# Kernel tuning notes

Hardware: AMD Instinct MI355X
Metric: run time of the kernel (lower is better)

Reference implementation:

```python
import jax, jax.numpy as jnp
import numpy as np

# corner enumeration order matches the original list comprehension:
# (0,0,0),(0,0,d),(0,h,0),(0,h,d),(w,0,0),(w,0,d),(w,h,0),(w,h,d)
CORNER_OFFS = jnp.array([[0,0,0],[0,0,1],[0,1,0],[0,1,1],
                         [1,0,0],[1,0,1],[1,1,0],[1,1,1]], dtype=jnp.float32)
# axis_combinations in original: (i,j) with j>=i over 3 axes -> 6 combos
CROSS_A = jnp.array([0,0,0,1,1,2])
CROSS_B = jnp.array([0,1,2,1,2,2])


def setup_inputs() -> dict:
    key = jax.random.key(0)
    k1, k2, k3 = jax.random.split(key, 3)
    B = 1024
    bb = jax.random.uniform(k1, (B, 6), dtype=jnp.float32)
    rotations = jax.random.normal(k2, (B, 3, 3), dtype=jnp.float32)
    translations = jax.random.normal(k3, (B, 1, 3), dtype=jnp.float32)
    return {"bb": bb, "rotations": rotations, "translations": translations}


def _pv_loss(bb, rotations, translations):
    B = bb.shape[0]
    # [B,8,3] axis-aligned corners, then rotate (corners @ R) and translate
    corners = bb[:, None, :3] + bb[:, None, 3:] * CORNER_OFFS
    corners_t = jnp.einsum('bkd,bde->bke', corners, rotations) + translations
    # unit_vectors is the 3x3 identity, so I @ R == R
    uvt = rotations  # [B,3,3] rows are the transformed unit vectors

    ii, jj = jnp.triu_indices(B, k=1)  # all pairs j > i, P = B(B-1)/2
    c1 = corners_t[ii]  # [P,8,3]
    c2 = corners_t[jj]  # [P,8,3]
    u1 = uvt[ii]        # [P,3,3]
    u2 = uvt[jj]        # [P,3,3]

    # NOTE: the original second axis-loop also uses unit_vector_first[i]
    # (a bug we replicate): the 3 face axes of the FIRST box are tested twice;
    # duplicates do not change min() or the all-intersect decision, so we test
    # them once. Cross axes use the j>=i combinations.
    face_axes = u1                                           # [P,3,3]
    cross_axes = jnp.cross(u1[:, CROSS_A, :], u2[:, CROSS_B, :])  # [P,6,3]
    axes = jnp.concatenate([face_axes, cross_axes], axis=1)  # [P,9,3]
    # original skips exactly-zero cross axes (torch.equal with zeros)
    valid = jnp.concatenate(
        [jnp.ones(face_axes.shape[:2], dtype=bool),
         jnp.any(cross_axes != 0, axis=-1)], axis=1)         # [P,9]

    # SAT projections: dot every corner with every axis
    d1 = jnp.einsum('pkc,pac->pak', c1, axes)  # [P,9,8]
    d2 = jnp.einsum('pkc,pac->pak', c2, axes)  # [P,9,8]
    min1, max1 = d1.min(-1), d1.max(-1)
    min2, max2 = d2.min(-1), d2.max(-1)
    total_len = jnp.maximum(max1, max2) - jnp.minimum(min1, min2)
    sum_len = (max1 - min1) + (max2 - min2)
    overlap = sum_len - total_len                 # [P,9]

    axis_pass = jnp.where(valid, total_len < sum_len, True)
    pair_pass = jnp.all(axis_pass, axis=-1)       # [P]
    overlap_masked = jnp.where(valid, overlap, jnp.inf)
    penalty = jnp.where(pair_pass, overlap_masked.min(-1), 0.0)
    return penalty.sum()


def reference(bb, rotations, translations):
    return _pv_loss(bb, rotations, translations)
```

## Files before the change

### kernel.cpp

```cpp
#include <hip/hip_runtime.h>
#include <hip/hip_bf16.h>

#define NI 8

__device__ __forceinline__ void load_box(const float* __restrict__ bb,
                                         const float* __restrict__ rot,
                                         const float* __restrict__ tr,
                                         int b, float* R, float* p, float* e) {
    const float* s = bb + b * 6;
    const float* r = rot + b * 9;
    const float* t = tr + b * 3;
    float mn0 = s[0], mn1 = s[1], mn2 = s[2];
    float d0 = s[3], d1 = s[4], d2 = s[5];
#pragma unroll
    for (int k = 0; k < 9; k++) R[k] = r[k];
#pragma unroll
    for (int k = 0; k < 3; k++) {
        p[k]     = mn0 * R[k] + mn1 * R[3 + k] + mn2 * R[6 + k] + t[k];
        e[k]     = d0 * R[k];
        e[3 + k] = d1 * R[3 + k];
        e[6 + k] = d2 * R[6 + k];
    }
}

__device__ __forceinline__ float axis_overlap(float ax, float ay, float az,
                                              const float* pi, const float* ei,
                                              const float* pj, const float* ej) {
    float b1 = pi[0] * ax + pi[1] * ay + pi[2] * az;
    float u0 = ei[0] * ax + ei[1] * ay + ei[2] * az;
    float u1 = ei[3] * ax + ei[4] * ay + ei[5] * az;
    float u2 = ei[6] * ax + ei[7] * ay + ei[8] * az;
    float s1 = b1 + 0.5f * (u0 + u1 + u2);
    float h1 = 0.5f * (fabsf(u0) + fabsf(u1) + fabsf(u2));

    float b2 = pj[0] * ax + pj[1] * ay + pj[2] * az;
    float v0 = ej[0] * ax + ej[1] * ay + ej[2] * az;
    float v1 = ej[3] * ax + ej[4] * ay + ej[5] * az;
    float v2 = ej[6] * ax + ej[7] * ay + ej[8] * az;
    float s2 = b2 + 0.5f * (v0 + v1 + v2);
    float h2 = 0.5f * (fabsf(v0) + fabsf(v1) + fabsf(v2));

    return fminf(s1 + h1, s2 + h2) - fmaxf(s1 - h1, s2 - h2);
}

__global__ __launch_bounds__(256) void pv_pairs(const float* __restrict__ bb,
                                                const float* __restrict__ rot,
                                                const float* __restrict__ tr,
                                                float* __restrict__ partial, int B) {
    const int jc = blockIdx.x;
    const int ic = blockIdx.y;
    const int jbase = jc * 256;
    const int ibase = ic * NI;
    const int j = jbase + threadIdx.x;

    float pen = 0.0f;
    if (ibase < jbase + 256 && j < B) {
        float Rj[9], pj[3], ej[9];
        load_box(bb, rot, tr, j, Rj, pj, ej);

#pragma unroll 2
        for (int ii = 0; ii < NI; ii++) {
            const int i = ibase + ii;
            if (i >= B) break;
            if (i >= j) continue;
            float Ri[9], pi[3], ei[9];
            load_box(bb, rot, tr, i, Ri, pi, ei);

            bool pass = true;
            float minov = __builtin_inff();

#pragma unroll
            for (int a = 0; a < 3; a++) {
                float ov = axis_overlap(Ri[a * 3], Ri[a * 3 + 1], Ri[a * 3 + 2],
                                        pi, ei, pj, ej);
                pass = pass && (ov > 0.0f);
                minov = fminf(minov, ov);
            }
            const int CA[6] = {0, 0, 0, 1, 1, 2};
            const int CB[6] = {0, 1, 2, 1, 2, 2};
#pragma unroll
            for (int c = 0; c < 6; c++) {
                const int ra = CA[c], rb = CB[c];
                float ux = Ri[ra * 3], uy = Ri[ra * 3 + 1], uz = Ri[ra * 3 + 2];
                float vx = Rj[rb * 3], vy = Rj[rb * 3 + 1], vz = Rj[rb * 3 + 2];
                float ax = uy * vz - uz * vy;
                float ay = uz * vx - ux * vz;
                float az = ux * vy - uy * vx;
                if ((ax != 0.0f) || (ay != 0.0f) || (az != 0.0f)) {
                    float ov = axis_overlap(ax, ay, az, pi, ei, pj, ej);
                    pass = pass && (ov > 0.0f);
                    minov = fminf(minov, ov);
                }
            }
            pen += pass ? minov : 0.0f;
        }
    }

#pragma unroll
    for (int off = 32; off > 0; off >>= 1) pen += __shfl_down(pen, off);
    __shared__ float wsum[4];
    const int wid = threadIdx.x >> 6;
    if ((threadIdx.x & 63) == 0) wsum[wid] = pen;
    __syncthreads();
    if (threadIdx.x == 0)
        partial[blockIdx.y * gridDim.x + blockIdx.x] = wsum[0] + wsum[1] + wsum[2] + wsum[3];
}

__global__ __launch_bounds__(256) void pv_reduce(const float* __restrict__ partial,
                                                 float* __restrict__ out, int n) {
    float s = 0.0f;
    for (int k = threadIdx.x; k < n; k += 256) s += partial[k];
#pragma unroll
    for (int off = 32; off > 0; off >>= 1) s += __shfl_down(s, off);
    __shared__ float wsum[4];
    const int wid = threadIdx.x >> 6;
    if ((threadIdx.x & 63) == 0) wsum[wid] = s;
    __syncthreads();
    if (threadIdx.x == 0) out[0] = wsum[0] + wsum[1] + wsum[2] + wsum[3];
}

extern "C" void kernel_launch(void* const* d_in, const int* in_sizes, int n_in,
                              void* d_out, int out_size, void* d_ws, size_t ws_size,
                              hipStream_t stream) {
    const float* bb  = (const float*)d_in[0];
    const float* rot = (const float*)d_in[1];
    const float* tr  = (const float*)d_in[2];
    float* out = (float*)d_out;
    const int B = in_sizes[0] / 6;

    float* partial = (float*)d_ws;

    const int gx = (B + 255) / 256;
    const int gy = (B + NI - 1) / NI;
    dim3 grid(gx, gy);
    dim3 block(256);
    pv_pairs<<<grid, block, 0, stream>>>(bb, rot, tr, partial, B);
    pv_reduce<<<1, 256, 0, stream>>>(partial, out, gx * gy);
}
```

Before: 76.24 us.

## Launch only triangular-valid pair blocks via 1D grid and shrink i-tile

Replaces the 2D grid, where about half the blocks exited immediately because they fell below the triangle, with a compact 1D grid that enumerates only blocks whose i-range overlaps the j-tile. Each block decodes its (jc, ic) with a short loop. NI is halved to 4 and the inner loop fully unrolled, which yields more, smaller blocks for better load balance. The cost is a small per-block index-decode loop and more partial sums for the reduce kernel to add.

```diff
diff --git a/kernel.cpp b/kernel.cpp
--- a/kernel.cpp
+++ b/kernel.cpp
@@ -1,7 +1,8 @@
 #include <hip/hip_runtime.h>
 #include <hip/hip_bf16.h>
 
-#define NI 8
+#define NI 4
+#define JT 256
 
 __device__ __forceinline__ void load_box(const float* __restrict__ bb,
                                          const float* __restrict__ rot,
@@ -43,22 +44,28 @@
     return fminf(s1 + h1, s2 + h2) - fmaxf(s1 - h1, s2 - h2);
 }
 
-__global__ __launch_bounds__(256) void pv_pairs(const float* __restrict__ bb,
-                                                const float* __restrict__ rot,
-                                                const float* __restrict__ tr,
-                                                float* __restrict__ partial, int B) {
-    const int jc = blockIdx.x;
-    const int ic = blockIdx.y;
-    const int jbase = jc * 256;
+__global__ __launch_bounds__(JT) void pv_pairs(const float* __restrict__ bb,
+                                               const float* __restrict__ rot,
+                                               const float* __restrict__ tr,
+                                               float* __restrict__ partial, int B) {
+    const int icAll = (B + NI - 1) / NI;
+    int bid = blockIdx.x;
+    int jc = 0, base = 0, ic = 0;
+    for (;; jc++) {
+        int icmax = min(((jc + 1) * JT + NI - 1) / NI, icAll);
+        if (bid < base + icmax) { ic = bid - base; break; }
+        base += icmax;
+    }
+    const int jbase = jc * JT;
     const int ibase = ic * NI;
     const int j = jbase + threadIdx.x;
 
     float pen = 0.0f;
-    if (ibase < jbase + 256 && j < B) {
+    if (j < B) {
         float Rj[9], pj[3], ej[9];
         load_box(bb, rot, tr, j, Rj, pj, ej);
 
-#pragma unroll 2
+#pragma unroll
         for (int ii = 0; ii < NI; ii++) {
             const int i = ibase + ii;
             if (i >= B) break;
@@ -98,12 +105,16 @@
 
 #pragma unroll
     for (int off = 32; off > 0; off >>= 1) pen += __shfl_down(pen, off);
-    __shared__ float wsum[4];
+    __shared__ float wsum[JT / 64];
     const int wid = threadIdx.x >> 6;
     if ((threadIdx.x & 63) == 0) wsum[wid] = pen;
     __syncthreads();
-    if (threadIdx.x == 0)
-        partial[blockIdx.y * gridDim.x + blockIdx.x] = wsum[0] + wsum[1] + wsum[2] + wsum[3];
+    if (threadIdx.x == 0) {
+        float s = 0.0f;
+#pragma unroll
+        for (int w = 0; w < JT / 64; w++) s += wsum[w];
+        partial[blockIdx.x] = s;
+    }
 }
 
 __global__ __launch_bounds__(256) void pv_reduce(const float* __restrict__ partial,
@@ -130,10 +141,14 @@
 
     float* partial = (float*)d_ws;
 
-    const int gx = (B + 255) / 256;
-    const int gy = (B + NI - 1) / NI;
-    dim3 grid(gx, gy);
-    dim3 block(256);
-    pv_pairs<<<grid, block, 0, stream>>>(bb, rot, tr, partial, B);
-    pv_reduce<<<1, 256, 0, stream>>>(partial, out, gx * gy);
+    const int gx = (B + JT - 1) / JT;
+    const int icAll = (B + NI - 1) / NI;
+    int total = 0;
+    for (int jc = 0; jc < gx; jc++) {
+        int icmax = ((jc + 1) * JT + NI - 1) / NI;
+        total += (icmax < icAll) ? icmax : icAll;
+    }
+
+    pv_pairs<<<dim3(total), dim3(JT), 0, stream>>>(bb, rot, tr, partial, B);
+    pv_reduce<<<1, 256, 0, stream>>>(partial, out, total);
 }
```

New measurement: 70.54 us. 7.5% less time.
